# Kernel optimization log

Measured on AMD Instinct MI355X. Metric: run time of the kernel, lower is better.

The kernel has to match this reference:

```python
import jax, jax.numpy as jnp
import numpy as np

B, IN_C, H, W = 2, 256, 128, 128
KQ = 128            # kq_dim
K_LOCAL = 5         # subsample_local_ksize -> 25 local samples
S = 32              # subsample_num_samples (25 local + 7 random global)
STRIDES = (1, 2, 4) # levels 2, 3, 4


def _local_inds(h, w, k):
    # create_local_ind_buffer: flat index of the KxK window around each pixel,
    # coordinates clamped at the border (padding by replication).
    off = np.arange(k) - k // 2
    ii = np.clip(np.arange(h)[:, None] + off[None, :], 0, h - 1)  # [h,k]
    jj = np.clip(np.arange(w)[:, None] + off[None, :], 0, w - 1)  # [w,k]
    inds = ii[:, None, :, None] * w + jj[None, :, None, :]        # [h,w,k,k]
    return inds.reshape(h * w, k * k)


def setup_inputs() -> dict:
    key = jax.random.key(0)
    ks = jax.random.split(key, 4)
    rng = np.random.RandomState(0)
    inp = {
        'feats': jax.random.normal(ks[0], (B, IN_C, H, W), jnp.float32),
        'conv_w': jax.random.normal(ks[1], (KQ, IN_C, 3, 3), jnp.float32) * 0.02,
        'conv_b': jnp.zeros((KQ,), jnp.float32),
        'key_w': jax.random.normal(ks[2], (KQ, KQ), jnp.float32) * 0.05,
        'key_b': jnp.zeros((KQ,), jnp.float32),
        'query_w': jax.random.normal(ks[3], (KQ, KQ), jnp.float32) * 0.05,
        'query_b': jnp.zeros((KQ,), jnp.float32),
    }
    for lvl, s in zip((2, 3, 4), STRIDES):
        h, w = H // s, W // s
        n = h * w
        loc = np.broadcast_to(_local_inds(h, w, K_LOCAL)[None], (B, n, K_LOCAL * K_LOCAL))
        glob = rng.randint(0, n, size=(B, n, S - K_LOCAL * K_LOCAL))
        inp['sample_inds_%d' % lvl] = jnp.asarray(np.concatenate([loc, glob], -1), jnp.int32)
    return inp


def _pool(x, s):
    # utils.downscale_tensor: average-pool by the level stride
    if s == 1:
        return x
    b, c, h, w = x.shape
    return x.reshape(b, c, h // s, s, w // s, s).mean(axis=(3, 5))


def _level_logits(key_f, query_f, stride, inds):
    k = _pool(key_f, stride)
    q = _pool(query_f, stride)
    b, c, h, w = k.shape
    k = k.reshape(b, c, h * w).transpose(0, 2, 1)   # [B,N,C]
    q = q.reshape(b, c, h * w).transpose(0, 2, 1)   # [B,N,C]
    gk = k[jnp.arange(b)[:, None, None], inds]      # gather keys -> [B,N,S,C]
    # (gathered_query * gathered_key).sum(-1); query gather at node_inds is identity
    return jnp.einsum('bnc,bnsc->bns', q, gk) * (c ** -0.5)


def reference(feats, conv_w, conv_b, key_w, key_b, query_w, query_b,
              sample_inds_2, sample_inds_3, sample_inds_4):
    x = jax.lax.conv_general_dilated(
        feats, conv_w, (1, 1), 'SAME',
        dimension_numbers=('NCHW', 'OIHW', 'NCHW')) + conv_b[None, :, None, None]
    keys = jnp.einsum('bchw,kc->bkhw', x, key_w) + key_b[None, :, None, None]
    queries = jnp.einsum('bchw,kc->bkhw', x, query_w) + query_b[None, :, None, None]
    logits = [
        _level_logits(keys, queries, s, i)
        for s, i in zip(STRIDES, (sample_inds_2, sample_inds_3, sample_inds_4))
    ]
    # subsample_logits for levels 2/3/4, concatenated along the node dim
    return jnp.concatenate(logits, axis=1)  # [B, 16384+4096+1024, S]
```

## Files before the change

### kernel.cpp

```cpp
#include <hip/hip_runtime.h>
#include <cstddef>
#include <cstdint>

typedef __attribute__((ext_vector_type(8))) short short8;
typedef __attribute__((ext_vector_type(4))) float f32x4;

namespace {
constexpr int B_   = 2;
constexpr int HW   = 16384;
constexpr int NTOT = 21504;
constexpr float SCALE = 0.088388347648318447f;
}

__device__ __forceinline__ unsigned short f2bf(float f) {
    unsigned u = __builtin_bit_cast(unsigned, f);
    u += 0x7fffu + ((u >> 16) & 1u);
    return (unsigned short)(u >> 16);
}
__device__ __forceinline__ float bf2f(unsigned short h) {
    return __builtin_bit_cast(float, (unsigned)h << 16);
}
__device__ __forceinline__ float blo(unsigned u) {
    return __builtin_bit_cast(float, u << 16);
}
__device__ __forceinline__ float bhi(unsigned u) {
    return __builtin_bit_cast(float, u & 0xffff0000u);
}
__device__ __forceinline__ unsigned pk2(float a, float b) {
    return (unsigned)f2bf(a) | ((unsigned)f2bf(b) << 16);
}
__device__ __forceinline__ void gload_lds16(const void* g, void* l) {
    __builtin_amdgcn_global_load_lds(
        (const __attribute__((address_space(1))) void*)g,
        (__attribute__((address_space(3))) void*)l, 16, 0, 0);
}

__global__ __launch_bounds__(256) void t2_k(
    const float* __restrict__ feats, unsigned short* __restrict__ fpm)
{
    const int tid = threadIdx.x;
    const int lane = tid & 63, cg = tid >> 6;
    const int y = blockIdx.x >> 1, xseg = blockIdx.x & 1;
    const int b = blockIdx.y;
    const int x = (xseg << 6) + lane;
    const bool inter = (y >= 1 && y <= 128);
    const float* src = feats + (((size_t)b * 256) << 14) + ((y - 1) << 7) + x;
    unsigned short* orow = fpm + ((size_t)(b * 130 + y) * 130 + 1 + x) * 256;

#pragma unroll
    for (int it = 0; it < 8; ++it) {
        const int c0 = (it << 5) + (cg << 3);
        uint4 v = {0u, 0u, 0u, 0u};
        if (inter) {
            float f0 = src[(size_t)(c0 + 0) << 14], f1 = src[(size_t)(c0 + 1) << 14];
            float f2 = src[(size_t)(c0 + 2) << 14], f3 = src[(size_t)(c0 + 3) << 14];
            float f4 = src[(size_t)(c0 + 4) << 14], f5 = src[(size_t)(c0 + 5) << 14];
            float f6 = src[(size_t)(c0 + 6) << 14], f7 = src[(size_t)(c0 + 7) << 14];
            v.x = pk2(f0, f1); v.y = pk2(f2, f3); v.z = pk2(f4, f5); v.w = pk2(f6, f7);
        }
        *(uint4*)(orow + c0) = v;
    }
    if (xseg == 0) {
        uint4 z = {0u, 0u, 0u, 0u};
        if (tid < 32)
            *(uint4*)(fpm + ((size_t)(b * 130 + y) * 130 + 0) * 256 + (tid << 3)) = z;
        else if (tid < 64)
            *(uint4*)(fpm + ((size_t)(b * 130 + y) * 130 + 129) * 256 + ((tid - 32) << 3)) = z;
    }
}

__global__ __launch_bounds__(256) void prep_k(
    const float* __restrict__ cw, const float* __restrict__ kw,
    const float* __restrict__ qw, const float* __restrict__ cb,
    const float* __restrict__ kb, const float* __restrict__ qb,
    unsigned short* __restrict__ wp, float* __restrict__ bias)
{
    const int tid = threadIdx.x;
    if (blockIdx.x == 576) {
        __shared__ float cbv[128];
        if (tid < 128) cbv[tid] = cb[tid];
        __syncthreads();
        const int oc = tid & 127, isQ = tid >> 7;
        const float* wrow = (isQ ? qw : kw) + oc * 128;
        float a = isQ ? qb[oc] : kb[oc];
        for (int j = 0; j < 128; ++j) a += wrow[j] * cbv[j];
        bias[tid] = a;
        return;
    }
    __shared__ float cvec[128][4];
    const int g = blockIdx.x;
    for (int idx = tid; idx < 512; idx += 256) {
        int j = idx >> 2, q = idx & 3;
        int pair = (g << 2) + q;
        int c = pair / 9, tap = pair - c * 9;
        cvec[j][q] = cw[j * 2304 + c * 9 + tap];
    }
    __syncthreads();
    const int oc = tid & 127, isQ = tid >> 7;
    const float* wrow = (isQ ? qw : kw) + oc * 128;
    float acc0 = 0.f, acc1 = 0.f, acc2 = 0.f, acc3 = 0.f;
    for (int j = 0; j < 128; ++j) {
        float wv = wrow[j];
        acc0 += wv * cvec[j][0]; acc1 += wv * cvec[j][1];
        acc2 += wv * cvec[j][2]; acc3 += wv * cvec[j][3];
    }
    float accs[4] = {acc0, acc1, acc2, acc3};
#pragma unroll
    for (int q = 0; q < 4; ++q) {
        int pair = (g << 2) + q;
        int c = pair / 9, tap = pair - c * 9;
        int chunk = c >> 5, kg = (c >> 3) & 3, i = c & 7;
        int nf = (isQ << 3) + (oc >> 4);
        int lane = (kg << 4) + (oc & 15);
        wp[((size_t)(((chunk * 9 + tap) << 4) + nf) << 9) + (lane << 3) + i] = f2bf(accs[q]);
    }
}

__global__ __launch_bounds__(256, 2) void conv3_k(
    const unsigned short* __restrict__ fpm, const unsigned short* __restrict__ wp,
    const float* __restrict__ kqbias, unsigned short* __restrict__ kT,
    unsigned short* __restrict__ qT, unsigned short* __restrict__ kT2,
    unsigned short* __restrict__ qT2, unsigned short* __restrict__ kT3,
    unsigned short* __restrict__ qT3)
{
    __shared__ __align__(16) unsigned char abuf[2][7168];
    __shared__ __align__(16) unsigned short obuf[64 * 264];

    const int tid = threadIdx.x;
    const int w = tid >> 6, lane = tid & 63;
    const int bid = blockIdx.x;
    const int b = bid >> 8, tile = bid & 255;
    const int ty0 = (tile >> 4) << 3, tx0 = (tile & 15) << 3;
    const int r = lane & 15, g = lane >> 4;

    const int sp_sub = lane >> 2, sp_o = (lane & 3) << 4;
    const int pbase = (((r >> 3) * 10) + (r & 7)) * 64 + (g << 4);
    const unsigned char* wpB = (const unsigned char*)wp + ((w << 2) << 10) + (lane << 4);

    f32x4 acc[4][4];
#pragma unroll
    for (int mi = 0; mi < 4; ++mi)
#pragma unroll
        for (int ni = 0; ni < 4; ++ni) acc[mi][ni] = (f32x4){0.f, 0.f, 0.f, 0.f};

    auto stage = [&](int chunk, int buf) {
#pragma unroll
        for (int k = 0; k < 2; ++k) {
            int i = w + (k << 2);
            if (i < 7) {
                int pl0 = (i << 4) + sp_sub;
                int y = (pl0 * 6554) >> 16;
                int x = pl0 - y * 10;
                const unsigned char* src = (const unsigned char*)fpm +
                    (((size_t)((b * 130 + ty0 + y) * 130 + tx0 + x)) << 9) +
                    (chunk << 6) + sp_o;
                gload_lds16(src, &abuf[buf][i << 10]);
            }
        }
    };

    stage(0, 0);
    __syncthreads();

    for (int chunk = 0; chunk < 8; ++chunk) {
        const unsigned char* ab = abuf[chunk & 1];
        if (chunk < 7) stage(chunk + 1, (chunk + 1) & 1);
        const unsigned char* wbase = wpB + (size_t)chunk * 147456;
#pragma unroll
        for (int tap = 0; tap < 9; ++tap) {
            const int dy = tap / 3, dx = tap % 3;
            short8 bf[4];
#pragma unroll
            for (int ni = 0; ni < 4; ++ni)
                bf[ni] = *(const short8*)(wbase + tap * 16384 + (ni << 10));
            short8 af[4];
#pragma unroll
            for (int mi = 0; mi < 4; ++mi)
                af[mi] = *(const short8*)(ab + pbase + (((2 * mi + dy) * 10 + dx) << 6));
#pragma unroll
            for (int mi = 0; mi < 4; ++mi)
#pragma unroll
                for (int ni = 0; ni < 4; ++ni)
                    acc[mi][ni] = __builtin_amdgcn_mfma_f32_16x16x32_bf16(
                        af[mi], bf[ni], acc[mi][ni], 0, 0, 0);
        }
        __syncthreads();
    }

    const int col = lane & 15;
    const int mrow0 = g << 2;
#pragma unroll
    for (int ni = 0; ni < 4; ++ni) {
        const int nf = (w << 2) + ni;
        const float bv = kqbias[(nf << 4) + col];
#pragma unroll
        for (int mi = 0; mi < 4; ++mi)
#pragma unroll
            for (int reg = 0; reg < 4; ++reg) {
                int m = mrow0 + reg;
                int pxl = ((2 * mi + (m >> 3)) << 3) + (m & 7);
                obuf[pxl * 264 + (nf << 4) + col] = f2bf(acc[mi][ni][reg] + bv);
            }
    }
    __syncthreads();

    {
        const int px = tid >> 2, q = tid & 3;
        const int gp = ((ty0 + (px >> 3)) << 7) + tx0 + (px & 7);
        const unsigned short* srow = obuf + px * 264 + (q << 6);
        unsigned short* dp = (q < 2)
            ? kT + ((((size_t)b << 14) + gp) << 7) + (q << 6)
            : qT + ((((size_t)b << 14) + gp) << 7) + ((q - 2) << 6);
#pragma unroll
        for (int j = 0; j < 8; ++j)
            *(uint4*)(dp + (j << 3)) = *(const uint4*)(srow + (j << 3));
    }

    {
        const int pp = tid >> 4, ocg = tid & 15, oc0 = ocg << 4;
        const int py2 = pp >> 2, px2 = pp & 3;
        const int gp2 = (((ty0 >> 1) + py2) << 6) + (tx0 >> 1) + px2;
        unsigned short* dp = (oc0 < 128)
            ? kT2 + (((size_t)b * 4096 + gp2) << 7) + oc0
            : qT2 + (((size_t)b * 4096 + gp2) << 7) + (oc0 - 128);
#pragma unroll
        for (int h = 0; h < 2; ++h) {
            float s0=0,s1=0,s2=0,s3=0,s4=0,s5=0,s6=0,s7=0;
#pragma unroll
            for (int dy = 0; dy < 2; ++dy)
#pragma unroll
                for (int dx = 0; dx < 2; ++dx) {
                    int pxl = (((py2 << 1) + dy) << 3) + (px2 << 1) + dx;
                    uint4 v = *(const uint4*)(obuf + pxl * 264 + oc0 + (h << 3));
                    s0 += blo(v.x); s1 += bhi(v.x); s2 += blo(v.y); s3 += bhi(v.y);
                    s4 += blo(v.z); s5 += bhi(v.z); s6 += blo(v.w); s7 += bhi(v.w);
                }
            uint4 o;
            o.x = pk2(s0 * 0.25f, s1 * 0.25f); o.y = pk2(s2 * 0.25f, s3 * 0.25f);
            o.z = pk2(s4 * 0.25f, s5 * 0.25f); o.w = pk2(s6 * 0.25f, s7 * 0.25f);
            *(uint4*)(dp + (h << 3)) = o;
        }
    }

    if (tid < 64) {
        const int pp = tid >> 4, ocg = tid & 15, oc0 = ocg << 4;
        const int py4 = pp >> 1, px4 = pp & 1;
        const int gp4 = (((ty0 >> 2) + py4) << 5) + (tx0 >> 2) + px4;
        unsigned short* dp = (oc0 < 128)
            ? kT3 + (((size_t)b * 1024 + gp4) << 7) + oc0
            : qT3 + (((size_t)b * 1024 + gp4) << 7) + (oc0 - 128);
#pragma unroll
        for (int h = 0; h < 2; ++h) {
            float s0=0,s1=0,s2=0,s3=0,s4=0,s5=0,s6=0,s7=0;
#pragma unroll
            for (int dy = 0; dy < 4; ++dy)
#pragma unroll
                for (int dx = 0; dx < 4; ++dx) {
                    int pxl = (((py4 << 2) + dy) << 3) + (px4 << 2) + dx;
                    uint4 v = *(const uint4*)(obuf + pxl * 264 + oc0 + (h << 3));
                    s0 += blo(v.x); s1 += bhi(v.x); s2 += blo(v.y); s3 += bhi(v.y);
                    s4 += blo(v.z); s5 += bhi(v.z); s6 += blo(v.w); s7 += bhi(v.w);
                }
            const float f = 0.0625f;
            uint4 o;
            o.x = pk2(s0 * f, s1 * f); o.y = pk2(s2 * f, s3 * f);
            o.z = pk2(s4 * f, s5 * f); o.w = pk2(s6 * f, s7 * f);
            *(uint4*)(dp + (h << 3)) = o;
        }
    }
}

__global__ __launch_bounds__(512) void gdot_all_k(
    const unsigned short* __restrict__ qT1, const unsigned short* __restrict__ kT1,
    const unsigned short* __restrict__ qT2, const unsigned short* __restrict__ kT2,
    const unsigned short* __restrict__ qT3, const unsigned short* __restrict__ kT3,
    const int* __restrict__ i2, const int* __restrict__ i3, const int* __restrict__ i4,
    float* __restrict__ out)
{
    __shared__ __align__(16) unsigned char kwin[144 * 256];

    const int raw = blockIdx.x;
    const int bid = (raw & 7) * 84 + (raw >> 3);

    const unsigned short *qT, *kT;
    const int* inds;
    int n, wshift, tpbsh, twsh, off;
    if (bid < 512) {
        qT = qT1; kT = kT1; inds = i2; n = 16384; wshift = 7; tpbsh = 8; twsh = 4; off = 0;
    } else if (bid < 640) {
        qT = qT2; kT = kT2; inds = i3; n = 4096;  wshift = 6; tpbsh = 6; twsh = 3; off = 16384;
    } else {
        qT = qT3; kT = kT3; inds = i4; n = 1024;  wshift = 5; tpbsh = 4; twsh = 2; off = 20480;
    }
    const int lb   = bid - ((bid < 512) ? 0 : (bid < 640) ? 512 : 640);
    const int b    = lb >> tpbsh;
    const int tile = lb & ((1 << tpbsh) - 1);
    const int ty0  = (tile >> twsh) << 3;
    const int tx0  = (tile & ((1 << twsh) - 1)) << 3;
    const int W    = 1 << wshift, Wm1 = W - 1;
    const int ry0  = ty0 - 2, cx0 = tx0 - 2;

    const int tid   = threadIdx.x;
    const int pxl   = tid >> 3;
    const int slice = tid & 7;
    const int py = pxl >> 3, px = pxl & 7;
    const int nid = ((ty0 + py) << wshift) + tx0 + px;

    for (int idx = tid; idx < 2304; idx += 512) {
        int slot = idx >> 4, w16 = idx & 15;
        int sy = ry0 + slot / 12, sx = cx0 + slot % 12;
        sy = min(max(sy, 0), Wm1); sx = min(max(sx, 0), Wm1);
        uint4 v = *(const uint4*)(kT + ((size_t)(b * n + (sy << wshift) + sx) * 128) + (w16 << 3));
        *(uint4*)&kwin[slot * 256 + ((w16 ^ (slot & 7)) << 4)] = v;
    }

    float qr[16];
    {
        const uint4* qp = (const uint4*)(qT + ((size_t)(b * n + nid) * 128) + (slice << 4));
        uint4 q0 = qp[0], q1 = qp[1];
        qr[0] = blo(q0.x); qr[1] = bhi(q0.x); qr[2] = blo(q0.y); qr[3] = bhi(q0.y);
        qr[4] = blo(q0.z); qr[5] = bhi(q0.z); qr[6] = blo(q0.w); qr[7] = bhi(q0.w);
        qr[8] = blo(q1.x); qr[9] = bhi(q1.x); qr[10] = blo(q1.y); qr[11] = bhi(q1.y);
        qr[12] = blo(q1.z); qr[13] = bhi(q1.z); qr[14] = blo(q1.w); qr[15] = bhi(q1.w);
    }
    __syncthreads();

    const int* irow = inds + ((size_t)(b * n + nid) << 5);
    int ia[32];
    {
        const int4* ip = (const int4*)irow;
#pragma unroll
        for (int j = 0; j < 8; ++j) {
            int4 v = ip[j];
            ia[4 * j] = v.x; ia[4 * j + 1] = v.y; ia[4 * j + 2] = v.z; ia[4 * j + 3] = v.w;
        }
    }

    uint4 rk0[7], rk1[7];
#pragma unroll
    for (int rr = 0; rr < 7; ++rr) {
        const uint4* kp = (const uint4*)(kT + (((size_t)(b * n + ia[25 + rr])) << 7) + (slice << 4));
        rk0[rr] = kp[0]; rk1[rr] = kp[1];
    }

    const int w2 = slice << 1;
    float res4[4] = {0.f, 0.f, 0.f, 0.f};
    float* orow = out + (((size_t)b * NTOT + off + nid) << 5);

#pragma unroll
    for (int s = 0; s < 32; ++s) {
        uint4 k0, k1;
        if (s < 25) {
            int ind = ia[s];
            int iy = ind >> wshift, ix = ind & Wm1;
            int slot = (iy - ry0) * 12 + (ix - cx0);
            int sw = slot & 7;
            const unsigned char* base2 = kwin + slot * 256;
            k0 = *(const uint4*)(base2 + ((w2 ^ sw) << 4));
            k1 = *(const uint4*)(base2 + (((w2 + 1) ^ sw) << 4));
        } else {
            k0 = rk0[s - 25]; k1 = rk1[s - 25];
        }
        float a = qr[0] * blo(k0.x) + qr[1] * bhi(k0.x)
                + qr[2] * blo(k0.y) + qr[3] * bhi(k0.y)
                + qr[4] * blo(k0.z) + qr[5] * bhi(k0.z)
                + qr[6] * blo(k0.w) + qr[7] * bhi(k0.w)
                + qr[8] * blo(k1.x) + qr[9] * bhi(k1.x)
                + qr[10] * blo(k1.y) + qr[11] * bhi(k1.y)
                + qr[12] * blo(k1.z) + qr[13] * bhi(k1.z)
                + qr[14] * blo(k1.w) + qr[15] * bhi(k1.w);
        a += __shfl_xor(a, 1);
        a += __shfl_xor(a, 2);
        a += __shfl_xor(a, 4);
        if ((s >> 2) == slice) res4[s & 3] = a * SCALE;
    }
    *(float4*)(orow + (slice << 2)) = *(const float4*)res4;
}

extern "C" void kernel_launch(void* const* d_in, const int* in_sizes, int n_in,
                              void* d_out, int out_size, void* d_ws, size_t ws_size,
                              hipStream_t stream)
{
    const float* feats = (const float*)d_in[0];
    const float* cw    = (const float*)d_in[1];
    const float* cb    = (const float*)d_in[2];
    const float* kw    = (const float*)d_in[3];
    const float* kb    = (const float*)d_in[4];
    const float* qw    = (const float*)d_in[5];
    const float* qb    = (const float*)d_in[6];
    const int*   i2    = (const int*)d_in[7];
    const int*   i3    = (const int*)d_in[8];
    const int*   i4    = (const int*)d_in[9];
    float* out = (float*)d_out;

    char* ws = (char*)d_ws;
    unsigned short* wp   = (unsigned short*)ws;
    float*          bias = (float*)(ws + 1179648);
    unsigned short* fpm  = (unsigned short*)(ws + 1180672);
    unsigned short* kT1  = (unsigned short*)(ws + 18624512);
    unsigned short* qT1  = kT1 + 4194304;
    unsigned short* kT2  = qT1 + 4194304;
    unsigned short* qT2  = kT2 + 1048576;
    unsigned short* kT3  = qT2 + 1048576;
    unsigned short* qT3  = kT3 + 262144;

    t2_k<<<dim3(260, 2), 256, 0, stream>>>(feats, fpm);
    prep_k<<<dim3(577), 256, 0, stream>>>(cw, kw, qw, cb, kb, qb, wp, bias);
    conv3_k<<<dim3(512), 256, 0, stream>>>(fpm, wp, bias, kT1, qT1,
                                           kT2, qT2, kT3, qT3);
    gdot_all_k<<<dim3(672), 512, 0, stream>>>(qT1, kT1, qT2, kT2, qT3, kT3,
                                              i2, i3, i4, out);
}
```

Baseline: 186.9 us.

## Triple-buffer conv input staging and fuse transpose with weight prep kernel

Merges the feature transpose/pad kernel and the weight/bias prep kernel into a single launch keyed on block index. The conv kernel switches from double to triple LDS buffering with a prefetch distance of two chunks, using explicit vmcnt waits plus barriers instead of full syncthreads. This is meant to hide global-to-LDS latency and cut one launch. Staging now loads 8 rows unconditionally, so it reads a few extra out-of-tile pixels and uses more LDS.

After: 178.1 us. 1.05x faster.

```diff
diff --git a/kernel.cpp b/kernel.cpp
--- a/kernel.cpp
+++ b/kernel.cpp
@@ -35,48 +35,53 @@
         (__attribute__((address_space(3))) void*)l, 16, 0, 0);
 }
 
-__global__ __launch_bounds__(256) void t2_k(
-    const float* __restrict__ feats, unsigned short* __restrict__ fpm)
-{
-    const int tid = threadIdx.x;
-    const int lane = tid & 63, cg = tid >> 6;
-    const int y = blockIdx.x >> 1, xseg = blockIdx.x & 1;
-    const int b = blockIdx.y;
-    const int x = (xseg << 6) + lane;
-    const bool inter = (y >= 1 && y <= 128);
-    const float* src = feats + (((size_t)b * 256) << 14) + ((y - 1) << 7) + x;
-    unsigned short* orow = fpm + ((size_t)(b * 130 + y) * 130 + 1 + x) * 256;
-
-#pragma unroll
-    for (int it = 0; it < 8; ++it) {
-        const int c0 = (it << 5) + (cg << 3);
-        uint4 v = {0u, 0u, 0u, 0u};
-        if (inter) {
-            float f0 = src[(size_t)(c0 + 0) << 14], f1 = src[(size_t)(c0 + 1) << 14];
-            float f2 = src[(size_t)(c0 + 2) << 14], f3 = src[(size_t)(c0 + 3) << 14];
-            float f4 = src[(size_t)(c0 + 4) << 14], f5 = src[(size_t)(c0 + 5) << 14];
-            float f6 = src[(size_t)(c0 + 6) << 14], f7 = src[(size_t)(c0 + 7) << 14];
-            v.x = pk2(f0, f1); v.y = pk2(f2, f3); v.z = pk2(f4, f5); v.w = pk2(f6, f7);
-        }
-        *(uint4*)(orow + c0) = v;
-    }
-    if (xseg == 0) {
-        uint4 z = {0u, 0u, 0u, 0u};
-        if (tid < 32)
-            *(uint4*)(fpm + ((size_t)(b * 130 + y) * 130 + 0) * 256 + (tid << 3)) = z;
-        else if (tid < 64)
-            *(uint4*)(fpm + ((size_t)(b * 130 + y) * 130 + 129) * 256 + ((tid - 32) << 3)) = z;
-    }
-}
-
-__global__ __launch_bounds__(256) void prep_k(
-    const float* __restrict__ cw, const float* __restrict__ kw,
-    const float* __restrict__ qw, const float* __restrict__ cb,
-    const float* __restrict__ kb, const float* __restrict__ qb,
+#define KBAR2() asm volatile("s_waitcnt vmcnt(2)\ns_barrier" ::: "memory")
+#define KBAR0() asm volatile("s_waitcnt vmcnt(0)\ns_barrier" ::: "memory")
+
+__global__ __launch_bounds__(256) void tp_k(
+    const float* __restrict__ feats, const float* __restrict__ cw,
+    const float* __restrict__ kw, const float* __restrict__ qw,
+    const float* __restrict__ cb, const float* __restrict__ kb,
+    const float* __restrict__ qb, unsigned short* __restrict__ fpm,
     unsigned short* __restrict__ wp, float* __restrict__ bias)
 {
+    const int bid = blockIdx.x;
     const int tid = threadIdx.x;
-    if (blockIdx.x == 576) {
+
+    if (bid < 520) {
+        const int b = bid >= 260;
+        const int rem = bid - b * 260;
+        const int y = rem >> 1, xseg = rem & 1;
+        const int lane = tid & 63, cg = tid >> 6;
+        const int x = (xseg << 6) + lane;
+        const bool inter = (y >= 1 && y <= 128);
+        const float* src = feats + (((size_t)b * 256) << 14) + ((y - 1) << 7) + x;
+        unsigned short* orow = fpm + ((size_t)(b * 130 + y) * 130 + 1 + x) * 256;
+
+#pragma unroll
+        for (int it = 0; it < 8; ++it) {
+            const int c0 = (it << 5) + (cg << 3);
+            uint4 v = {0u, 0u, 0u, 0u};
+            if (inter) {
+                float f0 = src[(size_t)(c0 + 0) << 14], f1 = src[(size_t)(c0 + 1) << 14];
+                float f2 = src[(size_t)(c0 + 2) << 14], f3 = src[(size_t)(c0 + 3) << 14];
+                float f4 = src[(size_t)(c0 + 4) << 14], f5 = src[(size_t)(c0 + 5) << 14];
+                float f6 = src[(size_t)(c0 + 6) << 14], f7 = src[(size_t)(c0 + 7) << 14];
+                v.x = pk2(f0, f1); v.y = pk2(f2, f3); v.z = pk2(f4, f5); v.w = pk2(f6, f7);
+            }
+            *(uint4*)(orow + c0) = v;
+        }
+        if (xseg == 0) {
+            uint4 z = {0u, 0u, 0u, 0u};
+            if (tid < 32)
+                *(uint4*)(fpm + ((size_t)(b * 130 + y) * 130 + 0) * 256 + (tid << 3)) = z;
+            else if (tid < 64)
+                *(uint4*)(fpm + ((size_t)(b * 130 + y) * 130 + 129) * 256 + ((tid - 32) << 3)) = z;
+        }
+        return;
+    }
+
+    if (bid == 1096) {
         __shared__ float cbv[128];
         if (tid < 128) cbv[tid] = cb[tid];
         __syncthreads();
@@ -87,8 +92,9 @@
         bias[tid] = a;
         return;
     }
+
     __shared__ float cvec[128][4];
-    const int g = blockIdx.x;
+    const int g = bid - 520;
     for (int idx = tid; idx < 512; idx += 256) {
         int j = idx >> 2, q = idx & 3;
         int pair = (g << 2) + q;
@@ -116,14 +122,14 @@
     }
 }
 
-__global__ __launch_bounds__(256, 2) void conv3_k(
+__global__ __launch_bounds__(256, 2) void conv4_k(
     const unsigned short* __restrict__ fpm, const unsigned short* __restrict__ wp,
     const float* __restrict__ kqbias, unsigned short* __restrict__ kT,
     unsigned short* __restrict__ qT, unsigned short* __restrict__ kT2,
     unsigned short* __restrict__ qT2, unsigned short* __restrict__ kT3,
     unsigned short* __restrict__ qT3)
 {
-    __shared__ __align__(16) unsigned char abuf[2][7168];
+    __shared__ __align__(16) unsigned char abuf[3][8192];
     __shared__ __align__(16) unsigned short obuf[64 * 264];
 
     const int tid = threadIdx.x;
@@ -147,24 +153,23 @@
 #pragma unroll
         for (int k = 0; k < 2; ++k) {
             int i = w + (k << 2);
-            if (i < 7) {
-                int pl0 = (i << 4) + sp_sub;
-                int y = (pl0 * 6554) >> 16;
-                int x = pl0 - y * 10;
-                const unsigned char* src = (const unsigned char*)fpm +
-                    (((size_t)((b * 130 + ty0 + y) * 130 + tx0 + x)) << 9) +
-                    (chunk << 6) + sp_o;
-                gload_lds16(src, &abuf[buf][i << 10]);
-            }
+            int pl0 = (i << 4) + sp_sub;
+            int y = (pl0 * 6554) >> 16;
+            int x = pl0 - y * 10;
+            const unsigned char* src = (const unsigned char*)fpm +
+                (((size_t)((b * 130 + ty0 + y) * 130 + tx0 + x)) << 9) +
+                (chunk << 6) + sp_o;
+            gload_lds16(src, &abuf[buf][i << 10]);
         }
     };
 
     stage(0, 0);
-    __syncthreads();
-
+    stage(1, 1);
+    KBAR2();
+
+#pragma unroll
     for (int chunk = 0; chunk < 8; ++chunk) {
-        const unsigned char* ab = abuf[chunk & 1];
-        if (chunk < 7) stage(chunk + 1, (chunk + 1) & 1);
+        const unsigned char* ab = abuf[chunk % 3];
         const unsigned char* wbase = wpB + (size_t)chunk * 147456;
 #pragma unroll
         for (int tap = 0; tap < 9; ++tap) {
@@ -184,7 +189,12 @@
                     acc[mi][ni] = __builtin_amdgcn_mfma_f32_16x16x32_bf16(
                         af[mi], bf[ni], acc[mi][ni], 0, 0, 0);
         }
-        __syncthreads();
+        if (chunk < 6) {
+            stage(chunk + 2, (chunk + 2) % 3);
+            KBAR2();
+        } else if (chunk == 6) {
+            KBAR0();
+        }
     }
 
     const int col = lane & 15;
@@ -404,9 +414,9 @@
     unsigned short* kT3  = qT2 + 1048576;
     unsigned short* qT3  = kT3 + 262144;
 
-    t2_k<<<dim3(260, 2), 256, 0, stream>>>(feats, fpm);
-    prep_k<<<dim3(577), 256, 0, stream>>>(cw, kw, qw, cb, kb, qb, wp, bias);
-    conv3_k<<<dim3(512), 256, 0, stream>>>(fpm, wp, bias, kT1, qT1,
+    tp_k<<<dim3(1097), 256, 0, stream>>>(feats, cw, kw, qw, cb, kb, qb,
+                                         fpm, wp, bias);
+    conv4_k<<<dim3(512), 256, 0, stream>>>(fpm, wp, bias, kT1, qT1,
                                            kT2, qT2, kT3, qT3);
     gdot_all_k<<<dim3(672), 512, 0, stream>>>(qT1, kT1, qT2, kT2, qT3, kT3,
                                               i2, i3, i4, out);
```
